# Performance work log

Hardware: AMD Instinct MI355X
Metric: run time of the kernel (lower is better)

The kernel has to match this reference:

```python
import jax, jax.numpy as jnp
import numpy as np

B, L, D, H, S, V, K = 2, 64, 1024, 512, 50000, 40000, 32
SLM_LOGITS_SCALE = 0.1
BN_EPS = 1e-5


def setup_inputs() -> dict:
    key = jax.random.key(0)
    ks = jax.random.split(key, 8)
    return {
        "cached_embeddings": jax.random.normal(ks[0], (B, L, D), dtype=jnp.float32),
        "bn_gamma": jnp.ones((L,), jnp.float32),
        "bn_beta": jnp.zeros((L,), jnp.float32),
        "W1": jax.random.normal(ks[1], (D, H), dtype=jnp.float32) * 0.02,
        "b1": jnp.zeros((H,), jnp.float32),
        "W2": jax.random.normal(ks[2], (H, S), dtype=jnp.float32) * 0.02,
        "b2": jnp.zeros((S,), jnp.float32),
        "W_slm": jax.random.normal(ks[3], (H, V), dtype=jnp.float32) * 0.02,
        "b_slm": jnp.zeros((V,), jnp.float32),
        # fixed degree k=32 with values 1/min(deg,k) = 1/32 (full-degree rows)
        "sl_weights": jnp.full((S, K), 1.0 / K, jnp.float32),
        "sl_idx": jax.random.randint(ks[4], (S, K), 0, V, dtype=jnp.int32),
    }


def reference(cached_embeddings, bn_gamma, bn_beta, W1, b1, W2, b2,
              W_slm, b_slm, sl_weights, sl_idx):
    x = cached_embeddings  # [B, L, D]
    # BatchNorm1d(win_size): channels are sequence positions; stats over (B, D)
    mean = jnp.mean(x, axis=(0, 2), keepdims=True)
    var = jnp.var(x, axis=(0, 2), keepdims=True)
    xn = (x - mean) * jax.lax.rsqrt(var + BN_EPS)
    x = xn * bn_gamma[None, :, None] + bn_beta[None, :, None]
    # DenseEncoder: hidden + sense logits
    h = jax.nn.relu(jnp.einsum('bld,dh->blh', x, W1) + b1)  # [B, L, H]
    y = jnp.einsum('blh,hs->bls', h, W2) + b2                # [B, L, S]
    # SLM head: lemma logits
    v = jnp.einsum('blh,hv->blv', h, W_slm) + b_slm          # [B, L, V]
    # sparse sense->lemma matmul == weighted bounded-degree gather-sum
    g = v[..., sl_idx]                                       # [B, L, S, K]
    slm_logits = jnp.einsum('blsk,sk->bls', g, sl_weights)   # [B, L, S]
    return y + slm_logits * SLM_LOGITS_SCALE
```

## Files before the change

### kernel.cpp

```cpp
#include <hip/hip_runtime.h>

#define LL 64
#define DD 1024
#define HH 512
#define SS 50000
#define VV 40000
#define KD 32
#define MM 128

typedef __bf16 bf16_t;
typedef __bf16 bf16x8 __attribute__((ext_vector_type(8)));
typedef __bf16 bf16x4 __attribute__((ext_vector_type(4)));
typedef __bf16 bf16x2 __attribute__((ext_vector_type(2)));
typedef float f32x4 __attribute__((ext_vector_type(4)));

__device__ __forceinline__ void async_ld16(const void* g, void* l) {
    __builtin_amdgcn_global_load_lds(
        (const __attribute__((address_space(1))) void*)g,
        (__attribute__((address_space(3))) void*)l, 16, 0, 0);
}

#define WAITV(N) asm volatile("s_waitcnt vmcnt(" #N ")" ::: "memory")

__global__ __launch_bounds__(256) void k_bn(const float* __restrict__ x,
        const float* __restrict__ gamma, const float* __restrict__ beta,
        bf16_t* __restrict__ xn) {
    int l = blockIdx.x;
    int t = threadIdx.x;
    int b = t >> 7;
    int d0 = (t & 127) << 3;
    const float* xp = x + (size_t)(b * LL + l) * DD + d0;
    float4 v0 = *(const float4*)xp;
    float4 v1 = *(const float4*)(xp + 4);
    float s  = v0.x + v0.y + v0.z + v0.w + v1.x + v1.y + v1.z + v1.w;
    float ss = v0.x*v0.x + v0.y*v0.y + v0.z*v0.z + v0.w*v0.w
             + v1.x*v1.x + v1.y*v1.y + v1.z*v1.z + v1.w*v1.w;
    #pragma unroll
    for (int off = 32; off > 0; off >>= 1) {
        s  += __shfl_xor(s, off);
        ss += __shfl_xor(ss, off);
    }
    __shared__ float red[8];
    int wv = t >> 6, ln = t & 63;
    if (ln == 0) { red[wv] = s; red[4 + wv] = ss; }
    __syncthreads();
    float tot  = red[0] + red[1] + red[2] + red[3];
    float tots = red[4] + red[5] + red[6] + red[7];
    float mean = tot * (1.0f / 2048.0f);
    float var  = tots * (1.0f / 2048.0f) - mean * mean;
    float rstd = rsqrtf(var + 1e-5f);
    float g   = gamma[l] * rstd;
    float ofs = beta[l] - mean * g;
    bf16x8 o;
    o[0] = (bf16_t)(v0.x * g + ofs);
    o[1] = (bf16_t)(v0.y * g + ofs);
    o[2] = (bf16_t)(v0.z * g + ofs);
    o[3] = (bf16_t)(v0.w * g + ofs);
    o[4] = (bf16_t)(v1.x * g + ofs);
    o[5] = (bf16_t)(v1.y * g + ofs);
    o[6] = (bf16_t)(v1.z * g + ofs);
    o[7] = (bf16_t)(v1.w * g + ofs);
    *(bf16x8*)(xn + (size_t)(b * LL + l) * DD + d0) = o;
}

__global__ __launch_bounds__(64) void k_gemm1(const bf16_t* __restrict__ xn,
        const float* __restrict__ W1, const float* __restrict__ b1,
        bf16_t* __restrict__ h) {
    int lane = threadIdx.x & 63;
    int c = lane & 15, q = lane >> 4;
    int tile = blockIdx.x;
    int tm = tile >> 5, tn = tile & 31;
    int col = tn * 16 + c;
    f32x4 acc = {};
    for (int kk = 0; kk < DD; kk += 32) {
        bf16x8 afr = *(const bf16x8*)(xn + (size_t)(tm * 16 + c) * DD + kk + q * 8);
        bf16x8 bfr;
        #pragma unroll
        for (int j = 0; j < 8; ++j)
            bfr[j] = (bf16_t)W1[(size_t)(kk + q * 8 + j) * HH + col];
        acc = __builtin_amdgcn_mfma_f32_16x16x32_bf16(afr, bfr, acc, 0, 0, 0);
    }
    float bias = b1[col];
    #pragma unroll
    for (int r = 0; r < 4; ++r) {
        int m = tm * 16 + q * 4 + r;
        float v = acc[r] + bias;
        h[(size_t)m * HH + col] = (bf16_t)(v > 0.f ? v : 0.f);
    }
}

__global__ __launch_bounds__(256) void k_gemm_v(const bf16_t* __restrict__ h,
        const float* __restrict__ Wslm, const float* __restrict__ bslm,
        bf16_t* __restrict__ vT) {
    __shared__ __align__(16) char smem[3][16384];
    int t = threadIdx.x;
    int wv = t >> 6, lane = t & 63;
    int c = lane & 15, q = lane >> 4;
    int nb = blockIdx.x * 64;
    int col = nb + wv * 16 + c;
    int r  = t >> 4, sg = t & 15;
    const float* gw0 = Wslm + (size_t)r        * VV + nb + sg * 4;
    const float* gw1 = Wslm + (size_t)(r + 16) * VV + nb + sg * 4;
    int g0i = t, g1i = t + 256;
    const bf16_t* gh0 = h + (size_t)(((g0i >> 6) << 4) + ((g0i >> 2) & 15)) * HH + (g0i & 3) * 8;
    const bf16_t* gh1 = h + (size_t)(((g1i >> 6) << 4) + ((g1i >> 2) & 15)) * HH + (g1i & 3) * 8;

    #define STAGE_V(buf, kk) do { \
        async_ld16(gw0 + (size_t)(kk) * VV, smem[buf] + (size_t)t * 16); \
        async_ld16(gw1 + (size_t)(kk) * VV, smem[buf] + (size_t)(t + 256) * 16); \
        async_ld16(gh0 + (kk), smem[buf] + 8192 + (size_t)t * 16); \
        async_ld16(gh1 + (kk), smem[buf] + 8192 + (size_t)(t + 256) * 16); \
    } while (0)

    STAGE_V(0, 0); STAGE_V(1, 32); STAGE_V(2, 64);
    f32x4 acc[8] = {};

    auto compute = [&](int cur) {
        const float*  wb = (const float*)smem[cur];
        const bf16_t* hb = (const bf16_t*)(smem[cur] + 8192);
        bf16x8 bfr;
        #pragma unroll
        for (int j = 0; j < 8; ++j)
            bfr[j] = (bf16_t)wb[(q * 8 + j) * 64 + wv * 16 + c];
        #pragma unroll
        for (int ms = 0; ms < 8; ++ms) {
            bf16x8 afr = *(const bf16x8*)(hb + (size_t)(ms * 64 + c * 4 + q) * 8);
            acc[ms] = __builtin_amdgcn_mfma_f32_16x16x32_bf16(afr, bfr, acc[ms], 0, 0, 0);
        }
    };

    #pragma unroll 1
    for (int step = 0; step < 13; ++step) {
        WAITV(8);
        __builtin_amdgcn_s_barrier();
        int cur = step % 3;
        compute(cur);
        __builtin_amdgcn_s_barrier();
        STAGE_V(cur, (step + 3) * 32);
    }
    WAITV(8); __builtin_amdgcn_s_barrier(); compute(1);
    WAITV(4); __builtin_amdgcn_s_barrier(); compute(2);
    WAITV(0); __builtin_amdgcn_s_barrier(); compute(0);

    float bias = bslm[col];
    #pragma unroll
    for (int ms = 0; ms < 8; ++ms) {
        bf16x4 o;
        #pragma unroll
        for (int rr = 0; rr < 4; ++rr) o[rr] = (bf16_t)(acc[ms][rr] + bias);
        *(bf16x4*)(vT + (size_t)col * MM + ms * 16 + q * 4) = o;
    }
    #undef STAGE_V
}

__global__ __launch_bounds__(256) void k_gather(const bf16_t* __restrict__ vT,
        const float* __restrict__ slw, const int* __restrict__ slidx,
        bf16_t* __restrict__ slm) {
    int t = threadIdx.x;
    int wv = t >> 6, lane = t & 63;
    int s = blockIdx.x * 4 + wv;
    int idv = slidx[(size_t)s * KD + (lane & 31)];
    float wgt = slw[(size_t)s * KD + (lane & 31)];
    unsigned int u[KD];
    #pragma unroll
    for (int k = 0; k < KD; ++k) {
        int id = __shfl(idv, k);
        u[k] = *(const unsigned int*)(vT + (size_t)id * MM + lane * 2);
    }
    float a0 = 0.f, a1 = 0.f;
    #pragma unroll
    for (int k = 0; k < KD; ++k) {
        float w = __shfl(wgt, k);
        a0 += w * __uint_as_float(u[k] << 16);
        a1 += w * __uint_as_float(u[k] & 0xffff0000u);
    }
    bf16x2 o;
    o[0] = (bf16_t)a0;
    o[1] = (bf16_t)a1;
    *(bf16x2*)(slm + (size_t)s * MM + lane * 2) = o;
}

__global__ __launch_bounds__(256) void k_gemm_y(const bf16_t* __restrict__ h,
        const float* __restrict__ W2, const float* __restrict__ b2,
        const bf16_t* __restrict__ slm, float* __restrict__ out) {
    __shared__ __align__(16) char smem[3][16384];
    int t = threadIdx.x;
    int wv = t >> 6, lane = t & 63;
    int c = lane & 15, q = lane >> 4;
    int nb = blockIdx.x * 64;
    int col = nb + wv * 16 + c;
    int r  = t >> 4, sg = t & 15;
    int sgc = nb + sg * 4;
    bool ok = (sgc + 4 <= SS);
    const float* gw0 = ok ? (W2 + (size_t)r        * SS + sgc) : W2;
    const float* gw1 = ok ? (W2 + (size_t)(r + 16) * SS + sgc) : W2;
    int g0i = t, g1i = t + 256;
    const bf16_t* gh0 = h + (size_t)(((g0i >> 6) << 4) + ((g0i >> 2) & 15)) * HH + (g0i & 3) * 8;
    const bf16_t* gh1 = h + (size_t)(((g1i >> 6) << 4) + ((g1i >> 2) & 15)) * HH + (g1i & 3) * 8;

    #define STAGE_Y(buf, kk) do { \
        async_ld16(gw0 + (size_t)(kk) * SS, smem[buf] + (size_t)t * 16); \
        async_ld16(gw1 + (size_t)(kk) * SS, smem[buf] + (size_t)(t + 256) * 16); \
        async_ld16(gh0 + (kk), smem[buf] + 8192 + (size_t)t * 16); \
        async_ld16(gh1 + (kk), smem[buf] + 8192 + (size_t)(t + 256) * 16); \
    } while (0)

    STAGE_Y(0, 0); STAGE_Y(1, 32); STAGE_Y(2, 64);
    f32x4 acc[8] = {};

    auto compute = [&](int cur) {
        const float*  wb = (const float*)smem[cur];
        const bf16_t* hb = (const bf16_t*)(smem[cur] + 8192);
        bf16x8 bfr;
        #pragma unroll
        for (int j = 0; j < 8; ++j)
            bfr[j] = (bf16_t)wb[(q * 8 + j) * 64 + wv * 16 + c];
        #pragma unroll
        for (int ms = 0; ms < 8; ++ms) {
            bf16x8 afr = *(const bf16x8*)(hb + (size_t)(ms * 64 + c * 4 + q) * 8);
            acc[ms] = __builtin_amdgcn_mfma_f32_16x16x32_bf16(afr, bfr, acc[ms], 0, 0, 0);
        }
    };

    #pragma unroll 1
    for (int step = 0; step < 13; ++step) {
        WAITV(8);
        __builtin_amdgcn_s_barrier();
        int cur = step % 3;
        compute(cur);
        __builtin_amdgcn_s_barrier();
        STAGE_Y(cur, (step + 3) * 32);
    }
    WAITV(8); __builtin_amdgcn_s_barrier(); compute(1);
    WAITV(4); __builtin_amdgcn_s_barrier(); compute(2);
    WAITV(0); __builtin_amdgcn_s_barrier(); compute(0);

    if (col < SS) {
        float bias = b2[col];
        #pragma unroll
        for (int ms = 0; ms < 8; ++ms) {
            bf16x4 sv = *(const bf16x4*)(slm + (size_t)col * MM + ms * 16 + q * 4);
            #pragma unroll
            for (int rr = 0; rr < 4; ++rr) {
                int m = ms * 16 + q * 4 + rr;
                out[(size_t)m * SS + col] = acc[ms][rr] + bias + 0.1f * (float)sv[rr];
            }
        }
    }
    #undef STAGE_Y
}

extern "C" void kernel_launch(void* const* d_in, const int* in_sizes, int n_in,
                              void* d_out, int out_size, void* d_ws, size_t ws_size,
                              hipStream_t stream) {
    const float* x     = (const float*)d_in[0];
    const float* gamma = (const float*)d_in[1];
    const float* beta  = (const float*)d_in[2];
    const float* W1    = (const float*)d_in[3];
    const float* b1    = (const float*)d_in[4];
    const float* W2    = (const float*)d_in[5];
    const float* b2    = (const float*)d_in[6];
    const float* Wslm  = (const float*)d_in[7];
    const float* bslm  = (const float*)d_in[8];
    const float* slw   = (const float*)d_in[9];
    const int*   slidx = (const int*)d_in[10];
    float* out = (float*)d_out;

    char* ws = (char*)d_ws;
    bf16_t* xn  = (bf16_t*)ws;
    bf16_t* h   = (bf16_t*)(ws + 262144);
    bf16_t* vT  = (bf16_t*)(ws + 393216);
    bf16_t* slm = (bf16_t*)(ws + 10633216);

    k_bn    <<<64,    256, 0, stream>>>(x, gamma, beta, xn);
    k_gemm1 <<<256,   64,  0, stream>>>(xn, W1, b1, h);
    k_gemm_v<<<625,   256, 0, stream>>>(h, Wslm, bslm, vT);
    k_gather<<<12500, 256, 0, stream>>>(vT, slw, slidx, slm);
    k_gemm_y<<<782,   256, 0, stream>>>(h, W2, b2, slm, out);
}
```

Measured before the change: 312.4 us.

## Fuse sparse lemma gather into sense GEMM epilogue and double-buffer pipelines

```diff
diff --git a/kernel.cpp b/kernel.cpp
--- a/kernel.cpp
+++ b/kernel.cpp
@@ -13,6 +13,7 @@
 typedef __bf16 bf16x4 __attribute__((ext_vector_type(4)));
 typedef __bf16 bf16x2 __attribute__((ext_vector_type(2)));
 typedef float f32x4 __attribute__((ext_vector_type(4)));
+typedef float f32x2 __attribute__((ext_vector_type(2)));
 
 __device__ __forceinline__ void async_ld16(const void* g, void* l) {
     __builtin_amdgcn_global_load_lds(
@@ -92,7 +93,7 @@
 __global__ __launch_bounds__(256) void k_gemm_v(const bf16_t* __restrict__ h,
         const float* __restrict__ Wslm, const float* __restrict__ bslm,
         bf16_t* __restrict__ vT) {
-    __shared__ __align__(16) char smem[3][16384];
+    __shared__ __align__(16) char smem[2][16384];
     int t = threadIdx.x;
     int wv = t >> 6, lane = t & 63;
     int c = lane & 15, q = lane >> 4;
@@ -102,8 +103,8 @@
     const float* gw0 = Wslm + (size_t)r        * VV + nb + sg * 4;
     const float* gw1 = Wslm + (size_t)(r + 16) * VV + nb + sg * 4;
     int g0i = t, g1i = t + 256;
-    const bf16_t* gh0 = h + (size_t)(((g0i >> 6) << 4) + ((g0i >> 2) & 15)) * HH + (g0i & 3) * 8;
-    const bf16_t* gh1 = h + (size_t)(((g1i >> 6) << 4) + ((g1i >> 2) & 15)) * HH + (g1i & 3) * 8;
+    const bf16_t* gh0 = h + (size_t)(((g0i >> 6) << 4) + (g0i & 15)) * HH + ((g0i >> 4) & 3) * 8;
+    const bf16_t* gh1 = h + (size_t)(((g1i >> 6) << 4) + (g1i & 15)) * HH + ((g1i >> 4) & 3) * 8;
 
     #define STAGE_V(buf, kk) do { \
         async_ld16(gw0 + (size_t)(kk) * VV, smem[buf] + (size_t)t * 16); \
@@ -112,7 +113,7 @@
         async_ld16(gh1 + (kk), smem[buf] + 8192 + (size_t)(t + 256) * 16); \
     } while (0)
 
-    STAGE_V(0, 0); STAGE_V(1, 32); STAGE_V(2, 64);
+    STAGE_V(0, 0); STAGE_V(1, 32);
     f32x4 acc[8] = {};
 
     auto compute = [&](int cur) {
@@ -124,23 +125,21 @@
             bfr[j] = (bf16_t)wb[(q * 8 + j) * 64 + wv * 16 + c];
         #pragma unroll
         for (int ms = 0; ms < 8; ++ms) {
-            bf16x8 afr = *(const bf16x8*)(hb + (size_t)(ms * 64 + c * 4 + q) * 8);
+            bf16x8 afr = *(const bf16x8*)(hb + (size_t)(ms * 64 + lane) * 8);
             acc[ms] = __builtin_amdgcn_mfma_f32_16x16x32_bf16(afr, bfr, acc[ms], 0, 0, 0);
         }
     };
 
     #pragma unroll 1
-    for (int step = 0; step < 13; ++step) {
-        WAITV(8);
-        __builtin_amdgcn_s_barrier();
-        int cur = step % 3;
-        compute(cur);
-        __builtin_amdgcn_s_barrier();
-        STAGE_V(cur, (step + 3) * 32);
-    }
-    WAITV(8); __builtin_amdgcn_s_barrier(); compute(1);
-    WAITV(4); __builtin_amdgcn_s_barrier(); compute(2);
-    WAITV(0); __builtin_amdgcn_s_barrier(); compute(0);
+    for (int step = 0; step < 14; ++step) {
+        WAITV(4);
+        __builtin_amdgcn_s_barrier();
+        compute(step & 1);
+        __builtin_amdgcn_s_barrier();
+        STAGE_V(step & 1, (step + 2) * 32);
+    }
+    WAITV(4); __builtin_amdgcn_s_barrier(); compute(0);
+    WAITV(0); __builtin_amdgcn_s_barrier(); compute(1);
 
     float bias = bslm[col];
     #pragma unroll
@@ -153,37 +152,11 @@
     #undef STAGE_V
 }
 
-__global__ __launch_bounds__(256) void k_gather(const bf16_t* __restrict__ vT,
-        const float* __restrict__ slw, const int* __restrict__ slidx,
-        bf16_t* __restrict__ slm) {
-    int t = threadIdx.x;
-    int wv = t >> 6, lane = t & 63;
-    int s = blockIdx.x * 4 + wv;
-    int idv = slidx[(size_t)s * KD + (lane & 31)];
-    float wgt = slw[(size_t)s * KD + (lane & 31)];
-    unsigned int u[KD];
-    #pragma unroll
-    for (int k = 0; k < KD; ++k) {
-        int id = __shfl(idv, k);
-        u[k] = *(const unsigned int*)(vT + (size_t)id * MM + lane * 2);
-    }
-    float a0 = 0.f, a1 = 0.f;
-    #pragma unroll
-    for (int k = 0; k < KD; ++k) {
-        float w = __shfl(wgt, k);
-        a0 += w * __uint_as_float(u[k] << 16);
-        a1 += w * __uint_as_float(u[k] & 0xffff0000u);
-    }
-    bf16x2 o;
-    o[0] = (bf16_t)a0;
-    o[1] = (bf16_t)a1;
-    *(bf16x2*)(slm + (size_t)s * MM + lane * 2) = o;
-}
-
 __global__ __launch_bounds__(256) void k_gemm_y(const bf16_t* __restrict__ h,
         const float* __restrict__ W2, const float* __restrict__ b2,
-        const bf16_t* __restrict__ slm, float* __restrict__ out) {
-    __shared__ __align__(16) char smem[3][16384];
+        const bf16_t* __restrict__ vT, const float* __restrict__ slw,
+        const int* __restrict__ slidx, float* __restrict__ out) {
+    __shared__ __align__(16) char smem[2][16384];
     int t = threadIdx.x;
     int wv = t >> 6, lane = t & 63;
     int c = lane & 15, q = lane >> 4;
@@ -195,8 +168,8 @@
     const float* gw0 = ok ? (W2 + (size_t)r        * SS + sgc) : W2;
     const float* gw1 = ok ? (W2 + (size_t)(r + 16) * SS + sgc) : W2;
     int g0i = t, g1i = t + 256;
-    const bf16_t* gh0 = h + (size_t)(((g0i >> 6) << 4) + ((g0i >> 2) & 15)) * HH + (g0i & 3) * 8;
-    const bf16_t* gh1 = h + (size_t)(((g1i >> 6) << 4) + ((g1i >> 2) & 15)) * HH + (g1i & 3) * 8;
+    const bf16_t* gh0 = h + (size_t)(((g0i >> 6) << 4) + (g0i & 15)) * HH + ((g0i >> 4) & 3) * 8;
+    const bf16_t* gh1 = h + (size_t)(((g1i >> 6) << 4) + (g1i & 15)) * HH + ((g1i >> 4) & 3) * 8;
 
     #define STAGE_Y(buf, kk) do { \
         async_ld16(gw0 + (size_t)(kk) * SS, smem[buf] + (size_t)t * 16); \
@@ -205,7 +178,7 @@
         async_ld16(gh1 + (kk), smem[buf] + 8192 + (size_t)(t + 256) * 16); \
     } while (0)
 
-    STAGE_Y(0, 0); STAGE_Y(1, 32); STAGE_Y(2, 64);
+    STAGE_Y(0, 0); STAGE_Y(1, 32);
     f32x4 acc[8] = {};
 
     auto compute = [&](int cur) {
@@ -217,33 +190,64 @@
             bfr[j] = (bf16_t)wb[(q * 8 + j) * 64 + wv * 16 + c];
         #pragma unroll
         for (int ms = 0; ms < 8; ++ms) {
-            bf16x8 afr = *(const bf16x8*)(hb + (size_t)(ms * 64 + c * 4 + q) * 8);
+            bf16x8 afr = *(const bf16x8*)(hb + (size_t)(ms * 64 + lane) * 8);
             acc[ms] = __builtin_amdgcn_mfma_f32_16x16x32_bf16(afr, bfr, acc[ms], 0, 0, 0);
         }
     };
 
     #pragma unroll 1
-    for (int step = 0; step < 13; ++step) {
-        WAITV(8);
-        __builtin_amdgcn_s_barrier();
-        int cur = step % 3;
-        compute(cur);
-        __builtin_amdgcn_s_barrier();
-        STAGE_Y(cur, (step + 3) * 32);
-    }
-    WAITV(8); __builtin_amdgcn_s_barrier(); compute(1);
-    WAITV(4); __builtin_amdgcn_s_barrier(); compute(2);
-    WAITV(0); __builtin_amdgcn_s_barrier(); compute(0);
-
+    for (int step = 0; step < 14; ++step) {
+        WAITV(4);
+        __builtin_amdgcn_s_barrier();
+        compute(step & 1);
+        __builtin_amdgcn_s_barrier();
+        STAGE_Y(step & 1, (step + 2) * 32);
+    }
+    WAITV(4); __builtin_amdgcn_s_barrier(); compute(0);
+    WAITV(0); __builtin_amdgcn_s_barrier(); compute(1);
+
+    float* slds = (float*)&smem[0][0];
+    __syncthreads();
+    int l31 = lane & 31;
+    #pragma unroll 1
+    for (int ssi = 0; ssi < 16; ++ssi) {
+        int s = nb + wv * 16 + ssi;
+        float a0 = 0.f, a1 = 0.f;
+        if (s < SS) {
+            int   idv = slidx[(size_t)s * KD + l31];
+            float wgt = slw[(size_t)s * KD + l31];
+            #pragma unroll 1
+            for (int half = 0; half < 2; ++half) {
+                unsigned u[16];
+                #pragma unroll
+                for (int k = 0; k < 16; ++k) {
+                    int id = __shfl(idv, half * 16 + k);
+                    u[k] = *(const unsigned*)(vT + (size_t)id * MM + lane * 2);
+                }
+                #pragma unroll
+                for (int k = 0; k < 16; ++k) {
+                    float w = __shfl(wgt, half * 16 + k);
+                    a0 += w * __uint_as_float(u[k] << 16);
+                    a1 += w * __uint_as_float(u[k] & 0xffff0000u);
+                }
+            }
+        }
+        int row = wv * 16 + ssi;
+        int widx = (lane * 2) ^ ((ssi & 7) << 2);
+        f32x2 wr2; wr2[0] = a0; wr2[1] = a1;
+        *(f32x2*)&slds[(size_t)row * 128 + widx] = wr2;
+    }
     if (col < SS) {
         float bias = b2[col];
+        int row = wv * 16 + c;
         #pragma unroll
         for (int ms = 0; ms < 8; ++ms) {
-            bf16x4 sv = *(const bf16x4*)(slm + (size_t)col * MM + ms * 16 + q * 4);
+            f32x4 sv = *(const f32x4*)&slds[(size_t)row * 128
+                                            + ((ms * 16 + q * 4) ^ ((c & 7) << 2))];
             #pragma unroll
             for (int rr = 0; rr < 4; ++rr) {
                 int m = ms * 16 + q * 4 + rr;
-                out[(size_t)m * SS + col] = acc[ms][rr] + bias + 0.1f * (float)sv[rr];
+                out[(size_t)m * SS + col] = acc[ms][rr] + bias + 0.1f * sv[rr];
             }
         }
     }
@@ -270,11 +274,9 @@
     bf16_t* xn  = (bf16_t*)ws;
     bf16_t* h   = (bf16_t*)(ws + 262144);
     bf16_t* vT  = (bf16_t*)(ws + 393216);
-    bf16_t* slm = (bf16_t*)(ws + 10633216);
-
-    k_bn    <<<64,    256, 0, stream>>>(x, gamma, beta, xn);
-    k_gemm1 <<<256,   64,  0, stream>>>(xn, W1, b1, h);
-    k_gemm_v<<<625,   256, 0, stream>>>(h, Wslm, bslm, vT);
-    k_gather<<<12500, 256, 0, stream>>>(vT, slw, slidx, slm);
-    k_gemm_y<<<782,   256, 0, stream>>>(h, W2, b2, slm, out);
-}
+
+    k_bn    <<<64,  256, 0, stream>>>(x, gamma, beta, xn);
+    k_gemm1 <<<256, 64,  0, stream>>>(xn, W1, b1, h);
+    k_gemm_v<<<625, 256, 0, stream>>>(h, Wslm, bslm, vT);
+    k_gemm_y<<<782, 256, 0, stream>>>(h, W2, b2, vT, slw, slidx, out);
+}
```

Result: slower. 332.6 us (+6.5%).
